# Kernel optimization log

Hardware: AMD Instinct MI355X
Metric: run time of the kernel (lower is better)

The kernel has to match this reference:

```python
import jax, jax.numpy as jnp
import numpy as np

N, M, B, L, C, H = 4096, 16384, 8, 96, 512, 8
Dh = C // H


def setup_inputs() -> dict:
    key0 = jax.random.key(0)
    ks = jax.random.split(key0, 8)
    query = jax.random.normal(ks[0], (N, C), dtype=jnp.float32)
    key_t = jax.random.normal(ks[1], (M, C), dtype=jnp.float32)
    value = jax.random.normal(ks[2], (M, C), dtype=jnp.float32)
    keys_per_batch = M // B  # 2048 local key indices per scene
    idx = jax.random.randint(ks[3], (N, L), 0, keys_per_batch)
    pad = jax.random.uniform(ks[4], (N, L)) < 0.1
    pad = pad.at[:, 0].set(False)
    index_pair = jnp.where(pad, -1, idx).astype(jnp.int64)
    query_batch_cnt = jnp.full((B,), N // B, dtype=jnp.int32)
    key_batch_cnt = jnp.full((B,), M // B, dtype=jnp.int32)
    index_pair_batch = jnp.repeat(jnp.arange(B, dtype=jnp.int64), N // B)
    in_proj_weight = jax.random.normal(ks[5], (3 * C, C), dtype=jnp.float32) * (1.0 / np.sqrt(C))
    in_proj_bias = jnp.zeros((3 * C,), dtype=jnp.float32)
    out_proj_weight = jax.random.normal(ks[6], (C, C), dtype=jnp.float32) * (1.0 / np.sqrt(C))
    out_proj_bias = jnp.zeros((C,), dtype=jnp.float32)
    return {
        "query": query, "key": key_t, "value": value,
        "index_pair": index_pair, "query_batch_cnt": query_batch_cnt,
        "key_batch_cnt": key_batch_cnt, "index_pair_batch": index_pair_batch,
        "in_proj_weight": in_proj_weight, "in_proj_bias": in_proj_bias,
        "out_proj_weight": out_proj_weight, "out_proj_bias": out_proj_bias,
    }


def reference(query, key, value, index_pair, query_batch_cnt, key_batch_cnt,
              index_pair_batch, in_proj_weight, in_proj_bias,
              out_proj_weight, out_proj_bias):
    n, c = query.shape
    l = index_pair.shape[1]
    scaling = float(Dh) ** -0.5
    # QKV projections (F.linear: x @ W.T + b)
    q = query @ in_proj_weight[:c].T + in_proj_bias[:c]
    k = key @ in_proj_weight[c:2 * c].T + in_proj_bias[c:2 * c]
    v = value @ in_proj_weight[2 * c:].T + in_proj_bias[2 * c:]
    q = (q * scaling).reshape(n, H, Dh)
    k = k.reshape(-1, H, Dh)
    v = v.reshape(-1, H, Dh)
    mask = index_pair < 0  # (N, L)
    # convert local per-batch key index to global index via exclusive cumsum of key counts
    offs = jnp.concatenate([jnp.zeros((1,), key_batch_cnt.dtype), jnp.cumsum(key_batch_cnt)[:-1]])
    gidx = jnp.where(mask, 0, index_pair + offs[index_pair_batch][:, None])  # (N, L)
    k_g = k[gidx]  # (N, L, H, Dh)
    attn = jnp.einsum('nhd,nlhd->nlh', q, k_g)
    attn = jnp.where(mask[:, :, None], -jnp.inf, attn)
    attn = jax.nn.softmax(attn, axis=1)  # softmax over neighbor dim L
    v_g = v[gidx]  # (N, L, H, Dh)
    out = jnp.einsum('nlh,nlhd->nhd', attn, v_g).reshape(n, c)
    out = out @ out_proj_weight.T + out_proj_bias
    return out, attn.sum(axis=-1) / H
```

## Files before the change

kernel.cpp:

```cpp
#include <hip/hip_runtime.h>
#include <hip/hip_fp16.h>
#include <cstdint>
#include <cstddef>

#define N_Q 4096
#define M_K 16384
#define LNB 96
#define CH  512
#define NH  8

typedef _Float16 half8  __attribute__((ext_vector_type(8)));
typedef _Float16 h2     __attribute__((ext_vector_type(2)));
typedef float    floatx4 __attribute__((ext_vector_type(4)));
typedef float    floatx2 __attribute__((ext_vector_type(2)));

union H8 { half8 v; h2 p[4]; };

__device__ __forceinline__ h2 cvt2(float a, float b) {
    return __builtin_bit_cast(h2, __builtin_amdgcn_cvt_pkrtz(a, b));
}

__device__ __forceinline__ void async16(const void* g, void* l) {
    __builtin_amdgcn_global_load_lds(
        (const __attribute__((address_space(1))) void*)g,
        (__attribute__((address_space(3))) void*)l, 16, 0, 0);
}

template<int CTRL>
__device__ __forceinline__ float dpp_addf(float x) {
    int xi = __builtin_bit_cast(int, x);
    int yi = __builtin_amdgcn_update_dpp(xi, xi, CTRL, 0xF, 0xF, false);
    return x + __builtin_bit_cast(float, yi);
}
__device__ __forceinline__ float octet_sum(float x) {
    x = dpp_addf<0x141>(x);
    x = dpp_addf<0x4E>(x);
    x = dpp_addf<0xB1>(x);
    return x;
}

__global__ void cvt_weights(const float* __restrict__ wIn, const float* __restrict__ wOut,
                            _Float16* __restrict__ dst) {
    const size_t i = (size_t)blockIdx.x * blockDim.x + threadIdx.x;
    const float4 v = (i < 196608) ? ((const float4*)wIn)[i]
                                  : ((const float4*)wOut)[i - 196608];
    h2 a = cvt2(v.x, v.y);
    h2 b = cvt2(v.z, v.w);
    *(h2*)&dst[i * 4]     = a;
    *(h2*)&dst[i * 4 + 2] = b;
}

template<int OUTF16, int TM, int AFP32>
__device__ __forceinline__ void gemm_body(
    const void* __restrict__ Ap, const _Float16* __restrict__ Bw,
    const float* __restrict__ bias, void* __restrict__ outp, float oscale,
    int bm, int bn)
{
    constexpr int MI = TM / 32;
    __shared__ alignas(16) _Float16 As[TM * 32];
    __shared__ alignas(16) _Float16 Bs[128 * 32];

    const int t    = threadIdx.x;
    const int lane = t & 63;
    const int wave = t >> 6;
    const int wm   = wave >> 1, wn = wave & 1;

    floatx4 acc[MI][4] = {};

    const int rowL = t >> 2;
    const int kcol = (t & 3) * 8;
    const _Float16* gB = Bw + (size_t)(bn * 128 + rowL) * CH + kcol;
    _Float16* lB = &Bs[rowL * 32 + kcol];

    const _Float16* gA16 = nullptr; _Float16* lA16 = nullptr;
    const float* gA32 = nullptr; _Float16* lA32 = nullptr;
    if constexpr (AFP32) {
        gA32 = (const float*)Ap + (size_t)(bm * TM + rowL) * CH + kcol;
        lA32 = &As[rowL * 32 + kcol];
    } else {
        gA16 = (const _Float16*)Ap + (size_t)(bm * TM + rowL) * CH + kcol;
        lA16 = &As[rowL * 32 + kcol];
    }

    const int r0 = lane & 15;
    const int ko = (lane >> 4) * 8;

    for (int kt = 0; kt < CH / 32; ++kt) {
        if constexpr (AFP32) {
            const float* ga = gA32 + kt * 32;
            float4 x0 = ((const float4*)ga)[0], x1 = ((const float4*)ga)[1];
            H8 o0;
            o0.p[0] = cvt2(x0.x, x0.y);
            o0.p[1] = cvt2(x0.z, x0.w);
            o0.p[2] = cvt2(x1.x, x1.y);
            o0.p[3] = cvt2(x1.z, x1.w);
            *(half8*)lA32 = o0.v;
        } else {
            const _Float16* a0 = gA16 + kt * 32;
            async16(a0, lA16);
        }
        const _Float16* b0 = gB + kt * 32;
        async16(b0,           lB);
        async16(b0 + 64 * CH, lB + 64 * 32);
        __syncthreads();

        half8 af[MI], bf[4];
        #pragma unroll
        for (int mi = 0; mi < MI; ++mi)
            af[mi] = *(const half8*)&As[(wm * (TM / 2) + mi * 16 + r0) * 32 + ko];
        #pragma unroll
        for (int ni = 0; ni < 4; ++ni)
            bf[ni] = *(const half8*)&Bs[(wn * 64 + ni * 16 + r0) * 32 + ko];
        #pragma unroll
        for (int mi = 0; mi < MI; ++mi)
            #pragma unroll
            for (int ni = 0; ni < 4; ++ni)
                acc[mi][ni] = __builtin_amdgcn_mfma_f32_16x16x32_f16(
                    af[mi], bf[ni], acc[mi][ni], 0, 0, 0);
        __syncthreads();
    }

    #pragma unroll
    for (int mi = 0; mi < MI; ++mi) {
        #pragma unroll
        for (int ni = 0; ni < 4; ++ni) {
            const int col = bn * 128 + wn * 64 + ni * 16 + (lane & 15);
            const float bv = bias[col];
            #pragma unroll
            for (int r = 0; r < 4; ++r) {
                const int row = bm * TM + wm * (TM / 2) + mi * 16 + (lane >> 4) * 4 + r;
                const float v = (acc[mi][ni][r] + bv) * oscale;
                if (OUTF16) ((_Float16*)outp)[(size_t)row * CH + col] = (_Float16)v;
                else        ((float*)outp)[(size_t)row * CH + col]    = v;
            }
        }
    }
}

template<int OUTF16, int TM, int AFP32>
__global__ __launch_bounds__(256) void gemm_k(
    const void* __restrict__ A, const _Float16* __restrict__ Bw,
    const float* __restrict__ bias, void* __restrict__ outp, float oscale)
{
    const int bid = blockIdx.x;
    const int x   = bid & 7;
    const int i   = bid >> 3;
    const int bn  = i & 3;
    const int bm  = x + 8 * (i >> 2);
    gemm_body<OUTF16, TM, AFP32>(A, Bw, bias, outp, oscale, bm, bn);
}

__global__ __launch_bounds__(512, 4) void proj_qkv(
    const float* __restrict__ query, const float* __restrict__ keyp,
    const float* __restrict__ valp, const _Float16* __restrict__ w16,
    const float* __restrict__ bIn, _Float16* __restrict__ q16,
    _Float16* __restrict__ k16, _Float16* __restrict__ v16)
{
    const int bid = blockIdx.x;
    const float* Af; const _Float16* W; const float* bias; _Float16* dst;
    float osc; int bm, cb;

    if (bid < 512) {
        const int x = bid & 7;
        const int i = bid >> 3;
        const int bn = i & 3;
        bm = x + 8 * (i >> 2);
        const int z = bn >> 1;
        cb = (bn & 1) * 256;
        Af   = z ? valp : keyp;
        W    = w16 + (size_t)(512 + bn * 256) * 512;
        bias = bIn + 512 + bn * 256;
        dst  = z ? v16 : k16;
        osc  = 1.0f;
    } else {
        const int x = bid & 7;
        const int j = (bid - 512) >> 3;
        const int bn = j & 1;
        bm = x + 8 * (j >> 1);
        cb = bn * 256;
        Af   = query;
        W    = w16 + (size_t)(bn * 256) * 512;
        bias = bIn + bn * 256;
        dst  = q16;
        osc  = 0.125f;
    }

    __shared__ alignas(16) float    As[128 * 32];
    __shared__ alignas(16) _Float16 Bs[256 * 32];

    const char* Ab = (const char*)Af;
    const char* Bb = (const char*)W;

    const int t    = threadIdx.x;
    const int lane = t & 63;
    const int wv   = t >> 6;
    const int wm   = wv >> 2;
    const int wn   = wv & 3;
    const int r0   = lane & 15;
    const int hi   = lane >> 4;

    floatx4 acc[4][4] = {};

    uint32_t aoff[2];
    #pragma unroll
    for (int q = 0; q < 2; ++q) {
        const int G   = q * 512 + t;
        const int row = G >> 3;
        const int g   = (G & 7) ^ (row & 7);
        aoff[q] = (uint32_t)((bm * 128 + row) * 2048 + g * 16);
    }
    uint32_t boff[2];
    #pragma unroll
    for (int q = 0; q < 2; ++q) {
        const int G     = q * 512 + t;
        const int super = G >> 3;
        const int sgg   = (G & 7) ^ (super & 7);
        const int row   = super * 2 + (sgg >> 2);
        const int g     = sgg & 3;
        boff[q] = (uint32_t)(row * 1024 + g * 16);
    }

    for (int kt = 0; kt < 16; ++kt) {
        #pragma unroll
        for (int q = 0; q < 2; ++q)
            async16(Ab + aoff[q] + kt * 128, (char*)As + (q * 512 + t) * 16);
        #pragma unroll
        for (int q = 0; q < 2; ++q)
            async16(Bb + boff[q] + kt * 64,  (char*)Bs + (q * 512 + t) * 16);
        __syncthreads();

        half8 af[4], bf[4];
        #pragma unroll
        for (int mi = 0; mi < 4; ++mi) {
            const int row = wm * 64 + mi * 16 + r0;
            const int swz = row & 7;
            const float4 x0 = *(const float4*)((const char*)As + row * 128 + (((hi * 2)     ^ swz) * 16));
            const float4 x1 = *(const float4*)((const char*)As + row * 128 + (((hi * 2 + 1) ^ swz) * 16));
            H8 o;
            o.p[0] = cvt2(x0.x, x0.y);
            o.p[1] = cvt2(x0.z, x0.w);
            o.p[2] = cvt2(x1.x, x1.y);
            o.p[3] = cvt2(x1.z, x1.w);
            af[mi] = o.v;
        }
        #pragma unroll
        for (int ni = 0; ni < 4; ++ni) {
            const int row   = wn * 64 + ni * 16 + r0;
            const int super = row >> 1;
            const int vv    = ((row & 1) * 4 + hi) ^ (super & 7);
            bf[ni] = *(const half8*)((const char*)Bs + super * 128 + vv * 16);
        }
        #pragma unroll
        for (int mi = 0; mi < 4; ++mi)
            #pragma unroll
            for (int ni = 0; ni < 4; ++ni)
                acc[mi][ni] = __builtin_amdgcn_mfma_f32_16x16x32_f16(
                    af[mi], bf[ni], acc[mi][ni], 0, 0, 0);
        __syncthreads();
    }

    #pragma unroll
    for (int mi = 0; mi < 4; ++mi) {
        #pragma unroll
        for (int ni = 0; ni < 4; ++ni) {
            const int lc  = wn * 64 + ni * 16 + r0;
            const int col = cb + lc;
            const float bv = bias[lc];
            #pragma unroll
            for (int r = 0; r < 4; ++r) {
                const int row = bm * 128 + wm * 64 + mi * 16 + hi * 4 + r;
                dst[(size_t)row * CH + col] = (_Float16)((acc[mi][ni][r] + bv) * osc);
            }
        }
    }
}

__global__ __launch_bounds__(256) void attn_kernel(
    const _Float16* __restrict__ q16, const _Float16* __restrict__ k16,
    const _Float16* __restrict__ v16, const int* __restrict__ ipair,
    const int* __restrict__ ibatch, const int* __restrict__ kcnt,
    _Float16* __restrict__ op16, float* __restrict__ aout)
{
    __shared__ uint32_t vmask[LNB];
    __shared__ float    pls[LNB * 9];
    __shared__ __half2  pph[LNB * 9];
    __shared__ float    part[4][CH];

    const int t = threadIdx.x;
    const int n = ((blockIdx.x & 7) << 9) | (blockIdx.x >> 3);

    if (t < LNB) {
        const int idx = ipair[(size_t)n * LNB + t];
        const int b   = ibatch[n];
        int off = 0;
        for (int i = 0; i < b; ++i) off += kcnt[i];
        const uint32_t vo = (uint32_t)((idx < 0 ? 0 : (idx + off)) * (CH * 2));
        vmask[t] = vo | (idx < 0 ? 0x80000000u : 0u);
    }
    __syncthreads();

    const int lane = t & 63, wv = t >> 6;
    const int h    = lane >> 3;
    const int l0   = wv * 24;

    {
        const half8 qv = *(const half8*)(q16 + (size_t)n * CH + lane * 8);
        H8 qu; qu.v = qv;
        const char* kbase = (const char*)k16 + lane * 16;
        const int4* vb = (const int4*)&vmask[l0];
        for (int g = 0; g < 3; ++g) {
            const int4 w0 = vb[2 * g], w1 = vb[2 * g + 1];
            uint32_t vm8[8] = {(uint32_t)w0.x, (uint32_t)w0.y, (uint32_t)w0.z, (uint32_t)w0.w,
                               (uint32_t)w1.x, (uint32_t)w1.y, (uint32_t)w1.z, (uint32_t)w1.w};
            #pragma unroll
            for (int j = 0; j < 8; ++j) {
                const uint32_t vms = __builtin_amdgcn_readfirstlane(vm8[j]);
                H8 ku; ku.v = *(const half8*)(kbase + (vms & 0x7fffffffu));
                float acc = 0.f;
                #pragma unroll
                for (int u = 0; u < 4; ++u)
                    acc = __builtin_amdgcn_fdot2(qu.p[u], ku.p[u], acc, false);
                acc = octet_sum(acc);
                if ((lane & 7) == 0)
                    pls[(l0 + g * 8 + j) * 9 + h] = (vms & 0x80000000u) ? -1e30f : acc;
            }
        }
    }
    __syncthreads();

    {
        const int hh = t >> 5, j = t & 31;
        const float v0 = pls[j * 9 + hh];
        const float v1 = pls[(j + 32) * 9 + hh];
        const float v2 = pls[(j + 64) * 9 + hh];
        float m = fmaxf(v0, fmaxf(v1, v2));
        #pragma unroll
        for (int s = 16; s >= 1; s >>= 1) m = fmaxf(m, __shfl_xor(m, s, 32));
        const float e0 = __expf(v0 - m), e1 = __expf(v1 - m), e2 = __expf(v2 - m);
        float ssum = e0 + e1 + e2;
        #pragma unroll
        for (int s = 16; s >= 1; s >>= 1) ssum += __shfl_xor(ssum, s, 32);
        const float rinv = 1.0f / ssum;
        const float p0 = e0 * rinv, p1 = e1 * rinv, p2 = e2 * rinv;
        pls[j * 9 + hh]        = p0;
        pls[(j + 32) * 9 + hh] = p1;
        pls[(j + 64) * 9 + hh] = p2;
        pph[j * 9 + hh]        = __half2half2(__float2half_rn(p0));
        pph[(j + 32) * 9 + hh] = __half2half2(__float2half_rn(p1));
        pph[(j + 64) * 9 + hh] = __half2half2(__float2half_rn(p2));
    }
    __syncthreads();

    if (t < LNB) {
        float s = 0.f;
        #pragma unroll
        for (int u = 0; u < NH; ++u) s += pls[t * 9 + u];
        aout[(size_t)n * LNB + t] = s * (1.0f / NH);
    }

    {
        float accf[8] = {};
        const char* vbase = (const char*)v16 + lane * 16;
        const int4* vb = (const int4*)&vmask[l0];
        const __half2 hz = __half2half2(__float2half_rn(0.f));
        for (int g = 0; g < 3; ++g) {
            const int4 w0 = vb[2 * g], w1 = vb[2 * g + 1];
            uint32_t vm8[8] = {(uint32_t)w0.x, (uint32_t)w0.y, (uint32_t)w0.z, (uint32_t)w0.w,
                               (uint32_t)w1.x, (uint32_t)w1.y, (uint32_t)w1.z, (uint32_t)w1.w};
            __half2 a0 = hz, a1 = hz, a2 = hz, a3 = hz;
            #pragma unroll
            for (int j = 0; j < 8; ++j) {
                const uint32_t vms = __builtin_amdgcn_readfirstlane(vm8[j]);
                const half8 vv = *(const half8*)(vbase + (vms & 0x7fffffffu));
                union { half8 v; __half2 q[4]; } vu; vu.v = vv;
                const __half2 pp = pph[(l0 + g * 8 + j) * 9 + h];
                a0 = __hfma2(pp, vu.q[0], a0);
                a1 = __hfma2(pp, vu.q[1], a1);
                a2 = __hfma2(pp, vu.q[2], a2);
                a3 = __hfma2(pp, vu.q[3], a3);
            }
            float2 f;
            f = __half22float2(a0); accf[0] += f.x; accf[1] += f.y;
            f = __half22float2(a1); accf[2] += f.x; accf[3] += f.y;
            f = __half22float2(a2); accf[4] += f.x; accf[5] += f.y;
            f = __half22float2(a3); accf[6] += f.x; accf[7] += f.y;
        }
        floatx4 lo, hi;
        #pragma unroll
        for (int u = 0; u < 4; ++u) { lo[u] = accf[u]; hi[u] = accf[u + 4]; }
        *(floatx4*)&part[wv][lane * 8]     = lo;
        *(floatx4*)&part[wv][lane * 8 + 4] = hi;
    }
    __syncthreads();

    {
        const int c = t * 2;
        floatx2 s = *(const floatx2*)&part[0][c];
        #pragma unroll
        for (int w = 1; w < 4; ++w) {
            floatx2 pw = *(const floatx2*)&part[w][c];
            s[0] += pw[0]; s[1] += pw[1];
        }
        h2 o; o[0] = (_Float16)s[0]; o[1] = (_Float16)s[1];
        *(h2*)&op16[(size_t)n * CH + c] = o;
    }
}

extern "C" void kernel_launch(void* const* d_in, const int* in_sizes, int n_in,
                              void* d_out, int out_size, void* d_ws, size_t ws_size,
                              hipStream_t stream)
{
    const float* query = (const float*)d_in[0];
    const float* key   = (const float*)d_in[1];
    const float* value = (const float*)d_in[2];
    const int*   ipair = (const int*)d_in[3];
    const int*   kcnt  = (const int*)d_in[5];
    const int*   ibat  = (const int*)d_in[6];
    const float* wIn   = (const float*)d_in[7];
    const float* bIn   = (const float*)d_in[8];
    const float* wOut  = (const float*)d_in[9];
    const float* bOut  = (const float*)d_in[10];

    float* out  = (float*)d_out;
    float* aout = out + (size_t)N_Q * CH;

    char* ws = (char*)d_ws;
    _Float16* w16  = (_Float16*)(ws);
    _Float16* wo16 = (_Float16*)(ws + 1572864);
    _Float16* q16  = (_Float16*)(ws + 2097152);
    _Float16* k16  = (_Float16*)(ws + 6291456);
    _Float16* v16  = (_Float16*)(ws + 23068672);
    _Float16* op16 = (_Float16*)(ws + 39845888);

    cvt_weights<<<1024, 256, 0, stream>>>(wIn, wOut, w16);

    proj_qkv<<<576, 512, 0, stream>>>(query, key, value, w16, bIn, q16, k16, v16);

    attn_kernel<<<4096, 256, 0, stream>>>(q16, k16, v16, ipair, ibat, kcnt, op16, aout);

    gemm_k<0, 64, 0><<<256, 256, 0, stream>>>(op16, wo16, bOut, d_out, 1.0f);
}
```

Measured before the change: 97.33 us.

## Widen QKV projection tiles to full 512 output columns per block

Each proj_qkv block now computes a 128x512 output tile instead of 128x256, so the fp32 activation tile is loaded and converted to fp16 once per row block rather than twice. The grid halves to 288 blocks, the per-wave accumulator doubles to 4x8 MFMA tiles, and the weight LDS buffer doubles. This removes redundant A-matrix traffic and conversion work. In exchange it raises register and LDS pressure (occupancy hint lowered to 2) and gives fewer blocks to spread across the CUs.

```diff
diff --git a/kernel.cpp b/kernel.cpp
--- a/kernel.cpp
+++ b/kernel.cpp
@@ -150,7 +150,7 @@
     gemm_body<OUTF16, TM, AFP32>(A, Bw, bias, outp, oscale, bm, bn);
 }
 
-__global__ __launch_bounds__(512, 4) void proj_qkv(
+__global__ __launch_bounds__(512, 2) void proj_qkv(
     const float* __restrict__ query, const float* __restrict__ keyp,
     const float* __restrict__ valp, const _Float16* __restrict__ w16,
     const float* __restrict__ bIn, _Float16* __restrict__ q16,
@@ -158,35 +158,21 @@
 {
     const int bid = blockIdx.x;
     const float* Af; const _Float16* W; const float* bias; _Float16* dst;
-    float osc; int bm, cb;
-
-    if (bid < 512) {
-        const int x = bid & 7;
-        const int i = bid >> 3;
-        const int bn = i & 3;
-        bm = x + 8 * (i >> 2);
-        const int z = bn >> 1;
-        cb = (bn & 1) * 256;
-        Af   = z ? valp : keyp;
-        W    = w16 + (size_t)(512 + bn * 256) * 512;
-        bias = bIn + 512 + bn * 256;
-        dst  = z ? v16 : k16;
-        osc  = 1.0f;
+    float osc; int bm;
+
+    if (bid < 128) {
+        bm = bid;
+        Af = keyp;  W = w16 + (size_t)512 * 512;  bias = bIn + 512;  dst = k16;  osc = 1.0f;
+    } else if (bid < 256) {
+        bm = bid - 128;
+        Af = valp;  W = w16 + (size_t)1024 * 512; bias = bIn + 1024; dst = v16;  osc = 1.0f;
     } else {
-        const int x = bid & 7;
-        const int j = (bid - 512) >> 3;
-        const int bn = j & 1;
-        bm = x + 8 * (j >> 1);
-        cb = bn * 256;
-        Af   = query;
-        W    = w16 + (size_t)(bn * 256) * 512;
-        bias = bIn + bn * 256;
-        dst  = q16;
-        osc  = 0.125f;
+        bm = bid - 256;
+        Af = query; W = w16;                      bias = bIn;        dst = q16;  osc = 0.125f;
     }
 
     __shared__ alignas(16) float    As[128 * 32];
-    __shared__ alignas(16) _Float16 Bs[256 * 32];
+    __shared__ alignas(16) _Float16 Bs[512 * 32];
 
     const char* Ab = (const char*)Af;
     const char* Bb = (const char*)W;
@@ -199,7 +185,7 @@
     const int r0   = lane & 15;
     const int hi   = lane >> 4;
 
-    floatx4 acc[4][4] = {};
+    floatx4 acc[4][8] = {};
 
     uint32_t aoff[2];
     #pragma unroll
@@ -209,9 +195,9 @@
         const int g   = (G & 7) ^ (row & 7);
         aoff[q] = (uint32_t)((bm * 128 + row) * 2048 + g * 16);
     }
-    uint32_t boff[2];
+    uint32_t boff[4];
     #pragma unroll
-    for (int q = 0; q < 2; ++q) {
+    for (int q = 0; q < 4; ++q) {
         const int G     = q * 512 + t;
         const int super = G >> 3;
         const int sgg   = (G & 7) ^ (super & 7);
@@ -225,11 +211,11 @@
         for (int q = 0; q < 2; ++q)
             async16(Ab + aoff[q] + kt * 128, (char*)As + (q * 512 + t) * 16);
         #pragma unroll
-        for (int q = 0; q < 2; ++q)
+        for (int q = 0; q < 4; ++q)
             async16(Bb + boff[q] + kt * 64,  (char*)Bs + (q * 512 + t) * 16);
         __syncthreads();
 
-        half8 af[4], bf[4];
+        half8 af[4], bf[8];
         #pragma unroll
         for (int mi = 0; mi < 4; ++mi) {
             const int row = wm * 64 + mi * 16 + r0;
@@ -244,8 +230,8 @@
             af[mi] = o.v;
         }
         #pragma unroll
-        for (int ni = 0; ni < 4; ++ni) {
-            const int row   = wn * 64 + ni * 16 + r0;
+        for (int ni = 0; ni < 8; ++ni) {
+            const int row   = wn * 128 + ni * 16 + r0;
             const int super = row >> 1;
             const int vv    = ((row & 1) * 4 + hi) ^ (super & 7);
             bf[ni] = *(const half8*)((const char*)Bs + super * 128 + vv * 16);
@@ -253,7 +239,7 @@
         #pragma unroll
         for (int mi = 0; mi < 4; ++mi)
             #pragma unroll
-            for (int ni = 0; ni < 4; ++ni)
+            for (int ni = 0; ni < 8; ++ni)
                 acc[mi][ni] = __builtin_amdgcn_mfma_f32_16x16x32_f16(
                     af[mi], bf[ni], acc[mi][ni], 0, 0, 0);
         __syncthreads();
@@ -262,10 +248,9 @@
     #pragma unroll
     for (int mi = 0; mi < 4; ++mi) {
         #pragma unroll
-        for (int ni = 0; ni < 4; ++ni) {
-            const int lc  = wn * 64 + ni * 16 + r0;
-            const int col = cb + lc;
-            const float bv = bias[lc];
+        for (int ni = 0; ni < 8; ++ni) {
+            const int col = wn * 128 + ni * 16 + r0;
+            const float bv = bias[col];
             #pragma unroll
             for (int r = 0; r < 4; ++r) {
                 const int row = bm * 128 + wm * 64 + mi * 16 + hi * 4 + r;
@@ -434,7 +419,7 @@
 
     cvt_weights<<<1024, 256, 0, stream>>>(wIn, wOut, w16);
 
-    proj_qkv<<<576, 512, 0, stream>>>(query, key, value, w16, bIn, q16, k16, v16);
+    proj_qkv<<<288, 512, 0, stream>>>(query, key, value, w16, bIn, q16, k16, v16);
 
     attn_kernel<<<4096, 256, 0, stream>>>(q16, k16, v16, ipair, ibat, kcnt, op16, aout);
 
```

Measured after the change: 114.2 us. 1.17x slower.
